# Performance work log

Hardware: AMD Instinct MI355X
Metric: run time of the kernel (lower is better)

## Reference

```python
import jax, jax.numpy as jnp
import numpy as np

INPUT_DIM = 2048
CLASSES = 1000
BATCH = 8192


def setup_inputs() -> dict:
    key = jax.random.key(0)
    kx, ky, kwx, kbx, kwy, kby = jax.random.split(key, 6)
    s_in = 1.0 / np.sqrt(INPUT_DIM)
    return {
        "x": jax.random.normal(kx, (BATCH, INPUT_DIM), dtype=jnp.float32),
        "y": jax.random.normal(ky, (BATCH, INPUT_DIM), dtype=jnp.float32),
        "Wx": jax.random.uniform(kwx, (CLASSES, INPUT_DIM), jnp.float32, -s_in, s_in),
        "bx": jax.random.uniform(kbx, (CLASSES,), jnp.float32, -s_in, s_in),
        "Wy": jax.random.uniform(kwy, (CLASSES, INPUT_DIM), jnp.float32, -s_in, s_in),
        "by": jax.random.uniform(kby, (CLASSES,), jnp.float32, -s_in, s_in),
    }


def _ds_combin_two(alpha1, alpha2, classes):
    # alpha1, alpha2: [B, C] Dirichlet params
    S1 = jnp.sum(alpha1, axis=1, keepdims=True)  # [B,1]
    S2 = jnp.sum(alpha2, axis=1, keepdims=True)
    b1 = (alpha1 - 1.0) / S1                      # belief masses [B,C]
    b2 = (alpha2 - 1.0) / S2
    u1 = classes / S1                             # uncertainty [B,1]
    u2 = classes / S2
    # bb_sum = sum_{i,j} b1_i b2_j = (sum b1)(sum b2); bb_diag = sum_i b1_i b2_i
    bb_sum = jnp.sum(b1, axis=1) * jnp.sum(b2, axis=1)   # [B]
    bb_diag = jnp.sum(b1 * b2, axis=1)                    # [B]
    C = (bb_sum - bb_diag)[:, None]                       # conflict [B,1]
    denom = 1.0 - C
    b_a = (b1 * b2 + b1 * u2 + b2 * u1) / denom           # [B,C]
    u_a = (u1 * u2) / denom                               # [B,1]
    S_a = classes / u_a                                   # [B,1]
    return b_a * S_a + 1.0                                # alpha_a [B,C]


def reference(x, y, Wx, bx, Wy, by):
    out_x = x @ Wx.T + bx                 # [B,C]
    out_y = y @ Wy.T + by
    alpha_x = jax.nn.softplus(out_x) + 1.0
    alpha_y = jax.nn.softplus(out_y) + 1.0
    alpha_a = _ds_combin_two(alpha_x, alpha_y, CLASSES)
    return (alpha_a, alpha_x, alpha_y)
```

## Files before the change

### kernel.cpp

```cpp
#include <hip/hip_runtime.h>
#include <hip/hip_bf16.h>
#include <math.h>

#define BATCH_N 8192
#define K_DIM   2048
#define CLS     1000

typedef __attribute__((ext_vector_type(8))) short short8;
typedef __attribute__((ext_vector_type(8))) unsigned short ushort8;
typedef __attribute__((ext_vector_type(4))) float floatx4;

static __device__ __forceinline__ float softplus_fast(float z) {
    return fmaxf(z, 0.f) + __logf(1.f + __expf(-fabsf(z)));
}


constexpr int NT = K_DIM / 32;

#define BARX  __builtin_amdgcn_s_barrier()
#define LGKM0 asm volatile("s_waitcnt lgkmcnt(0)" ::: "memory")
#define SB0   __builtin_amdgcn_sched_barrier(0)
#define PRIO1 __builtin_amdgcn_s_setprio(1)
#define PRIO0 __builtin_amdgcn_s_setprio(0)

__global__ __launch_bounds__(512, 2)
void gemm_fused(const float* __restrict__ Xa, const float* __restrict__ Xb,
                const float* __restrict__ Wa, const float* __restrict__ Wb,
                const float* __restrict__ biasa, const float* __restrict__ biasb,
                float* __restrict__ outa, float* __restrict__ outb)
{
    int flat = blockIdx.x + 4 * (blockIdx.y + 32 * blockIdx.z);
    int sw   = (flat & 7) * 32 + (flat >> 3);
    const int bx = sw & 3, by = (sw >> 2) & 31, bz = sw >> 7;

    const float* A    = bz ? Xb : Xa;
    const float* B    = bz ? Wb : Wa;
    const float* bias = bz ? biasb : biasa;
    float* out        = bz ? outb : outa;

    __shared__ ushort As[2][256 * 32];
    __shared__ ushort Bs[2][256 * 32];

    const int tid  = threadIdx.x;
    const int lane = tid & 63;
    const int wid  = tid >> 6;
    const int wr = wid >> 2, wc = wid & 3;
    const int fr = lane & 15, fg = lane >> 4;
    const int brow = by * 256;
    const int bcol = bx * 256;

    size_t a_g[2], b_g[2];
    int    l_of[2];
#pragma unroll
    for (int i = 0; i < 2; ++i) {
        int q = tid + i * 512;
        int p = q >> 3, c8 = q & 7, c8l = c8 ^ (p & 7);
        int r = 2 * p + (c8l >> 2);
        int k = (c8l & 3) * 8;
        a_g[i] = (size_t)(brow + r) * K_DIM + k;
        int wrow = bcol + r; if (wrow >= CLS) wrow = CLS - 1;
        b_g[i] = (size_t)wrow * K_DIM + k;
        l_of[i] = q * 8;
    }

    int afoff[8], bfoff[4];
#pragma unroll
    for (int m = 0; m < 8; ++m) {
        int row = wr * 128 + m * 16 + fr;
        int p = row >> 1;
        int c = (((row & 1) << 2) | fg) ^ (p & 7);
        afoff[m] = (p * 8 + c) * 8;
    }
#pragma unroll
    for (int n = 0; n < 4; ++n) {
        int row = wc * 64 + n * 16 + fr;
        int p = row >> 1;
        int c = (((row & 1) << 2) | fg) ^ (p & 7);
        bfoff[n] = (p * 8 + c) * 8;
    }

    floatx4 acc[8][4];
#pragma unroll
    for (int m = 0; m < 8; ++m)
#pragma unroll
        for (int n = 0; n < 4; ++n)
            acc[m][n] = (floatx4){0.f, 0.f, 0.f, 0.f};

    float4 ga[2][2], gb[2][2];

#define LOADT(t_) {                                                           \
    const size_t kb_ = (size_t)(t_) * 32;                                     \
    ga[0][0] = *(const float4*)(A + a_g[0] + kb_);                            \
    ga[0][1] = *(const float4*)(A + a_g[0] + kb_ + 4);                        \
    ga[1][0] = *(const float4*)(A + a_g[1] + kb_);                            \
    ga[1][1] = *(const float4*)(A + a_g[1] + kb_ + 4);                        \
    gb[0][0] = *(const float4*)(B + b_g[0] + kb_);                            \
    gb[0][1] = *(const float4*)(B + b_g[0] + kb_ + 4);                        \
    gb[1][0] = *(const float4*)(B + b_g[1] + kb_);                            \
    gb[1][1] = *(const float4*)(B + b_g[1] + kb_ + 4);                        \
}

#define CVTW(sl_) {                                                           \
    _Pragma("unroll")                                                         \
    for (int i = 0; i < 2; ++i) {                                             \
        ushort8 ta, tb;                                                       \
        _Pragma("unroll")                                                     \
        for (int j = 0; j < 4; ++j) {                                         \
            ta[j]     = __hip_bfloat16_raw(__float2bfloat16(((const float*)&ga[i][0])[j])).x; \
            ta[j + 4] = __hip_bfloat16_raw(__float2bfloat16(((const float*)&ga[i][1])[j])).x; \
            tb[j]     = __hip_bfloat16_raw(__float2bfloat16(((const float*)&gb[i][0])[j])).x; \
            tb[j + 4] = __hip_bfloat16_raw(__float2bfloat16(((const float*)&gb[i][1])[j])).x; \
        }                                                                     \
        *(ushort8*)&As[sl_][l_of[i]] = ta;                                    \
        *(ushort8*)&Bs[sl_][l_of[i]] = tb;                                    \
    }                                                                         \
}

    LOADT(0)
    CVTW(0)
    LOADT(1)
    SB0; LGKM0; BARX; SB0;

#pragma unroll 1
    for (int t = 0; t < NT; ++t) {
        const ushort* asl = &As[t & 1][0];
        const ushort* bsl = &Bs[t & 1][0];
        short8 af[8], bf[4];
#pragma unroll
        for (int m = 0; m < 8; ++m) af[m] = *(const short8*)(asl + afoff[m]);
#pragma unroll
        for (int n = 0; n < 4; ++n) bf[n] = *(const short8*)(bsl + bfoff[n]);

        PRIO1;
#pragma unroll
        for (int m = 0; m < 8; ++m)
#pragma unroll
            for (int n = 0; n < 4; ++n)
                acc[m][n] = __builtin_amdgcn_mfma_f32_16x16x32_bf16(
                    af[m], bf[n], acc[m][n], 0, 0, 0);
        PRIO0;

        if (t + 1 < NT) CVTW((t + 1) & 1)
        if (t + 2 < NT) LOADT(t + 2)
        SB0; LGKM0; BARX; SB0;
    }

#pragma unroll
    for (int n = 0; n < 4; ++n) {
        int col = bcol + wc * 64 + n * 16 + fr;
        if (col >= CLS) continue;
        float bv = bias[col];
#pragma unroll
        for (int m = 0; m < 8; ++m) {
#pragma unroll
            for (int j = 0; j < 4; ++j) {
                int row = brow + wr * 128 + m * 16 + fg * 4 + j;
                float z = acc[m][n][j] + bv;
                out[(size_t)row * CLS + col] = softplus_fast(z) + 1.f;
            }
        }
    }
}


__global__ __launch_bounds__(256)
void ds_combine(const float* __restrict__ AX, const float* __restrict__ AY,
                float* __restrict__ out)
{
    const int row = blockIdx.x * 4 + (threadIdx.x >> 6);
    const int l = threadIdx.x & 63;
    const float* ax = AX + (size_t)row * CLS;
    const float* ay = AY + (size_t)row * CLS;

    float4 vx[4], vy[4];
    float sx = 0.f, sy = 0.f, sp = 0.f;
#pragma unroll
    for (int c = 0; c < 4; ++c) {
        int idx = l + c * 64;
        if (idx < CLS / 4) {
            vx[c] = *(const float4*)(ax + idx * 4);
            vy[c] = *(const float4*)(ay + idx * 4);
            const float* px = (const float*)&vx[c];
            const float* py = (const float*)&vy[c];
#pragma unroll
            for (int j = 0; j < 4; ++j) {
                sx += px[j]; sy += py[j];
                sp += (px[j] - 1.f) * (py[j] - 1.f);
            }
        }
    }
#pragma unroll
    for (int off = 1; off < 64; off <<= 1) {
        sx += __shfl_xor(sx, off);
        sy += __shfl_xor(sy, off);
        sp += __shfl_xor(sp, off);
    }
    const float S1 = sx, S2 = sy, P = sp;
    const float i1 = 1.f / S1, i2 = 1.f / S2;
    const float u1 = (float)CLS * i1, u2 = (float)CLS * i2;
    const float sb1 = (S1 - (float)CLS) * i1;
    const float sb2 = (S2 - (float)CLS) * i2;
    const float conf = sb1 * sb2 - P * i1 * i2;
    const float denom = 1.f - conf;
    const float idenom = 1.f / denom;
    const float Sa = (float)CLS * denom / (u1 * u2);

#pragma unroll
    for (int c = 0; c < 4; ++c) {
        int idx = l + c * 64;
        if (idx < CLS / 4) {
            float4 vo;
            const float* px = (const float*)&vx[c];
            const float* py = (const float*)&vy[c];
            float* po = (float*)&vo;
#pragma unroll
            for (int j = 0; j < 4; ++j) {
                float b1 = (px[j] - 1.f) * i1;
                float b2 = (py[j] - 1.f) * i2;
                float ba = (b1 * b2 + b1 * u2 + b2 * u1) * idenom;
                po[j] = ba * Sa + 1.f;
            }
            *(float4*)(out + (size_t)row * CLS + idx * 4) = vo;
        }
    }
}

extern "C" void kernel_launch(void* const* d_in, const int* in_sizes, int n_in,
                              void* d_out, int out_size, void* d_ws, size_t ws_size,
                              hipStream_t stream) {
    const float* x  = (const float*)d_in[0];
    const float* y  = (const float*)d_in[1];
    const float* Wx = (const float*)d_in[2];
    const float* bx = (const float*)d_in[3];
    const float* Wy = (const float*)d_in[4];
    const float* by = (const float*)d_in[5];
    float* out = (float*)d_out;
    float* ax = out + (size_t)BATCH_N * CLS;
    float* ay = ax  + (size_t)BATCH_N * CLS;

    gemm_fused<<<dim3(4, 32, 2), 512, 0, stream>>>(
        x, y, Wx, Wy, bx, by, ax, ay);
    ds_combine<<<BATCH_N / 4, 256, 0, stream>>>(ax, ay, out);
}
```

Measured before the change: 109.8 us.

## Pre-convert weights to swizzled bf16 image and stream B via direct global-to-LDS loads

```diff
diff --git a/kernel.cpp b/kernel.cpp
--- a/kernel.cpp
+++ b/kernel.cpp
@@ -14,14 +14,197 @@
     return fmaxf(z, 0.f) + __logf(1.f + __expf(-fabsf(z)));
 }
 
-
-constexpr int NT = K_DIM / 32;
+static __device__ __forceinline__ void gld_lds16(const void* g, void* l) {
+    __builtin_amdgcn_global_load_lds(
+        (const __attribute__((address_space(1))) void*)g,
+        (__attribute__((address_space(3))) void*)l, 16, 0, 0);
+}
+
+static __device__ __forceinline__ ushort f2bfr(float f) {
+    return __hip_bfloat16_raw(__float2bfloat16(f)).x;
+}
 
 #define BARX  __builtin_amdgcn_s_barrier()
 #define LGKM0 asm volatile("s_waitcnt lgkmcnt(0)" ::: "memory")
+#define VMW(n) asm volatile("s_waitcnt vmcnt(" #n ")" ::: "memory")
 #define SB0   __builtin_amdgcn_sched_barrier(0)
 #define PRIO1 __builtin_amdgcn_s_setprio(1)
 #define PRIO0 __builtin_amdgcn_s_setprio(0)
+
+constexpr int NT = K_DIM / 32;
+
+__global__ __launch_bounds__(256)
+void make_wimg(const float* __restrict__ wx, const float* __restrict__ wy,
+               ushort* __restrict__ imgx, ushort* __restrict__ imgy)
+{
+    const float* src = blockIdx.z ? wy : wx;
+    ushort* dst      = blockIdx.z ? imgy : imgx;
+    int c = blockIdx.x * 256 + threadIdx.x;
+    int q  = c & 1023;
+    int t  = (c >> 10) & 63;
+    int bx = c >> 16;
+    int p = q >> 3, c8 = q & 7, c8l = c8 ^ (p & 7);
+    int r = 2 * p + (c8l >> 2);
+    int k = (c8l & 3) * 8 + t * 32;
+    int row = bx * 256 + r;
+    ushort8 v = (ushort8)0;
+    if (row < CLS) {
+        float4 a = *(const float4*)(src + (size_t)row * K_DIM + k);
+        float4 b = *(const float4*)(src + (size_t)row * K_DIM + k + 4);
+#pragma unroll
+        for (int j = 0; j < 4; ++j) {
+            v[j]     = f2bfr(((const float*)&a)[j]);
+            v[j + 4] = f2bfr(((const float*)&b)[j]);
+        }
+    }
+    *(ushort8*)(dst + (size_t)c * 8) = v;
+}
+
+__global__ __launch_bounds__(512, 2)
+void gemm_fused2(const float* __restrict__ Xa, const float* __restrict__ Xb,
+                 const ushort* __restrict__ imgx, const ushort* __restrict__ imgy,
+                 const float* __restrict__ biasa, const float* __restrict__ biasb,
+                 float* __restrict__ outa, float* __restrict__ outb)
+{
+    int flat = blockIdx.x + 4 * (blockIdx.y + 32 * blockIdx.z);
+    int sw   = (flat & 7) * 32 + (flat >> 3);
+    const int bx = sw & 3, by = (sw >> 2) & 31, bz = sw >> 7;
+
+    const float* A     = bz ? Xb : Xa;
+    const ushort* Wimg = bz ? imgy : imgx;
+    const float* bias  = bz ? biasb : biasa;
+    float* out         = bz ? outb : outa;
+
+    __shared__ ushort As[2][256 * 32];
+    __shared__ ushort Bs[2][256 * 32];
+
+    const int tid  = threadIdx.x;
+    const int lane = tid & 63;
+    const int wid  = tid >> 6;
+    const int wr = wid >> 2, wc = wid & 3;
+    const int fr = lane & 15, fg = lane >> 4;
+    const int brow = by * 256;
+    const int bcol = bx * 256;
+
+    size_t a_g[2];
+    int    l_of[2];
+#pragma unroll
+    for (int i = 0; i < 2; ++i) {
+        int q = tid + i * 512;
+        int p = q >> 3, c8 = q & 7, c8l = c8 ^ (p & 7);
+        int r = 2 * p + (c8l >> 2);
+        a_g[i] = (size_t)(brow + r) * K_DIM + (c8l & 3) * 8;
+        l_of[i] = q * 8;
+    }
+    const ushort* wbase = Wimg + (size_t)bx * 64 * 1024 * 8;
+
+    int afoff[8], bfoff[4];
+#pragma unroll
+    for (int m = 0; m < 8; ++m) {
+        int row = wr * 128 + m * 16 + fr;
+        int p = row >> 1;
+        int c = (((row & 1) << 2) | fg) ^ (p & 7);
+        afoff[m] = (p * 8 + c) * 8;
+    }
+#pragma unroll
+    for (int n = 0; n < 4; ++n) {
+        int row = wc * 64 + n * 16 + fr;
+        int p = row >> 1;
+        int c = (((row & 1) << 2) | fg) ^ (p & 7);
+        bfoff[n] = (p * 8 + c) * 8;
+    }
+
+    floatx4 acc[8][4];
+#pragma unroll
+    for (int m = 0; m < 8; ++m)
+#pragma unroll
+        for (int n = 0; n < 4; ++n)
+            acc[m][n] = (floatx4){0.f, 0.f, 0.f, 0.f};
+
+    float4 ga[2][2];
+
+#define LOADT(t_) {                                                           \
+    const size_t kb_ = (size_t)(t_) * 32;                                     \
+    ga[0][0] = *(const float4*)(A + a_g[0] + kb_);                            \
+    ga[0][1] = *(const float4*)(A + a_g[0] + kb_ + 4);                        \
+    ga[1][0] = *(const float4*)(A + a_g[1] + kb_);                            \
+    ga[1][1] = *(const float4*)(A + a_g[1] + kb_ + 4);                        \
+}
+
+#define CVTW(sl_) {                                                           \
+    _Pragma("unroll")                                                         \
+    for (int i = 0; i < 2; ++i) {                                             \
+        ushort8 ta;                                                           \
+        _Pragma("unroll")                                                     \
+        for (int j = 0; j < 4; ++j) {                                         \
+            ta[j]     = f2bfr(((const float*)&ga[i][0])[j]);                  \
+            ta[j + 4] = f2bfr(((const float*)&ga[i][1])[j]);                  \
+        }                                                                     \
+        *(ushort8*)&As[sl_][l_of[i]] = ta;                                    \
+    }                                                                         \
+}
+
+#define STAGE_B(t_) {                                                         \
+    const ushort* s_ = wbase + (size_t)(t_) * 1024 * 8;                       \
+    gld_lds16(s_ + (size_t)tid * 8,         &Bs[(t_) & 1][tid * 8]);          \
+    gld_lds16(s_ + (size_t)(tid + 512) * 8, &Bs[(t_) & 1][(tid + 512) * 8]); \
+}
+
+    STAGE_B(0)
+    LOADT(0)
+    CVTW(0)
+    LOADT(1)
+    VMW(8);
+    LGKM0; BARX; SB0;
+
+#pragma unroll 1
+    for (int t = 0; t < NT; ++t) {
+        if (t + 1 < NT) STAGE_B(t + 1)
+        SB0;
+
+        const ushort* asl = &As[t & 1][0];
+        const ushort* bsl = &Bs[t & 1][0];
+        short8 af[8], bf[4];
+#pragma unroll
+        for (int m = 0; m < 8; ++m) af[m] = *(const short8*)(asl + afoff[m]);
+#pragma unroll
+        for (int n = 0; n < 4; ++n) bf[n] = *(const short8*)(bsl + bfoff[n]);
+
+        PRIO1;
+#pragma unroll
+        for (int m = 0; m < 8; ++m)
+#pragma unroll
+            for (int n = 0; n < 4; ++n)
+                acc[m][n] = __builtin_amdgcn_mfma_f32_16x16x32_bf16(
+                    af[m], bf[n], acc[m][n], 0, 0, 0);
+        PRIO0;
+
+        if (t + 1 < NT) CVTW((t + 1) & 1)
+        if (t + 2 < NT) LOADT(t + 2)
+        SB0;
+        if (t + 1 < NT) {
+            if (t + 2 < NT) { VMW(8); }
+            else           { VMW(0); }
+            LGKM0; BARX; SB0;
+        }
+    }
+
+#pragma unroll
+    for (int n = 0; n < 4; ++n) {
+        int col = bcol + wc * 64 + n * 16 + fr;
+        if (col >= CLS) continue;
+        float bv = bias[col];
+#pragma unroll
+        for (int m = 0; m < 8; ++m) {
+#pragma unroll
+            for (int j = 0; j < 4; ++j) {
+                int row = brow + wr * 128 + m * 16 + fg * 4 + j;
+                float z = acc[m][n][j] + bv;
+                out[(size_t)row * CLS + col] = softplus_fast(z) + 1.f;
+            }
+        }
+    }
+}
 
 __global__ __launch_bounds__(512, 2)
 void gemm_fused(const float* __restrict__ Xa, const float* __restrict__ Xb,
@@ -88,7 +271,7 @@
 
     float4 ga[2][2], gb[2][2];
 
-#define LOADT(t_) {                                                           \
+#define FLOADT(t_) {                                                          \
     const size_t kb_ = (size_t)(t_) * 32;                                     \
     ga[0][0] = *(const float4*)(A + a_g[0] + kb_);                            \
     ga[0][1] = *(const float4*)(A + a_g[0] + kb_ + 4);                        \
@@ -99,26 +282,25 @@
     gb[1][0] = *(const float4*)(B + b_g[1] + kb_);                            \
     gb[1][1] = *(const float4*)(B + b_g[1] + kb_ + 4);                        \
 }
-
-#define CVTW(sl_) {                                                           \
+#define FCVTW(sl_) {                                                          \
     _Pragma("unroll")                                                         \
     for (int i = 0; i < 2; ++i) {                                             \
         ushort8 ta, tb;                                                       \
         _Pragma("unroll")                                                     \
         for (int j = 0; j < 4; ++j) {                                         \
-            ta[j]     = __hip_bfloat16_raw(__float2bfloat16(((const float*)&ga[i][0])[j])).x; \
-            ta[j + 4] = __hip_bfloat16_raw(__float2bfloat16(((const float*)&ga[i][1])[j])).x; \
-            tb[j]     = __hip_bfloat16_raw(__float2bfloat16(((const float*)&gb[i][0])[j])).x; \
-            tb[j + 4] = __hip_bfloat16_raw(__float2bfloat16(((const float*)&gb[i][1])[j])).x; \
+            ta[j]     = f2bfr(((const float*)&ga[i][0])[j]);                  \
+            ta[j + 4] = f2bfr(((const float*)&ga[i][1])[j]);                  \
+            tb[j]     = f2bfr(((const float*)&gb[i][0])[j]);                  \
+            tb[j + 4] = f2bfr(((const float*)&gb[i][1])[j]);                  \
         }                                                                     \
         *(ushort8*)&As[sl_][l_of[i]] = ta;                                    \
         *(ushort8*)&Bs[sl_][l_of[i]] = tb;                                    \
     }                                                                         \
 }
 
-    LOADT(0)
-    CVTW(0)
-    LOADT(1)
+    FLOADT(0)
+    FCVTW(0)
+    FLOADT(1)
     SB0; LGKM0; BARX; SB0;
 
 #pragma unroll 1
@@ -140,8 +322,8 @@
                     af[m], bf[n], acc[m][n], 0, 0, 0);
         PRIO0;
 
-        if (t + 1 < NT) CVTW((t + 1) & 1)
-        if (t + 2 < NT) LOADT(t + 2)
+        if (t + 1 < NT) FCVTW((t + 1) & 1)
+        if (t + 2 < NT) FLOADT(t + 2)
         SB0; LGKM0; BARX; SB0;
     }
 
@@ -238,7 +420,18 @@
     float* ax = out + (size_t)BATCH_N * CLS;
     float* ay = ax  + (size_t)BATCH_N * CLS;
 
-    gemm_fused<<<dim3(4, 32, 2), 512, 0, stream>>>(
-        x, y, Wx, Wy, bx, by, ax, ay);
+    const size_t IMG = (size_t)4 * 64 * 1024 * 8;
+    const size_t need = 2 * IMG * sizeof(ushort);
+
+    if (ws_size >= need) {
+        ushort* imgx = (ushort*)d_ws;
+        ushort* imgy = imgx + IMG;
+        make_wimg<<<dim3(1024, 1, 2), 256, 0, stream>>>(Wx, Wy, imgx, imgy);
+        gemm_fused2<<<dim3(4, 32, 2), 512, 0, stream>>>(
+            x, y, imgx, imgy, bx, by, ax, ay);
+    } else {
+        gemm_fused<<<dim3(4, 32, 2), 512, 0, stream>>>(
+            x, y, Wx, Wy, bx, by, ax, ay);
+    }
     ds_combine<<<BATCH_N / 4, 256, 0, stream>>>(ax, ay, out);
 }
```

After: 132.3 us. +20.5%, slower.

## Deepen GEMM LDS pipeline to four stages with one barrier per two tiles

Applied to the files above, without the earlier changes.

```diff
diff --git a/kernel.cpp b/kernel.cpp
--- a/kernel.cpp
+++ b/kernel.cpp
@@ -14,14 +14,18 @@
     return fmaxf(z, 0.f) + __logf(1.f + __expf(-fabsf(z)));
 }
 
-
-constexpr int NT = K_DIM / 32;
+static __device__ __forceinline__ ushort f2bfr(float f) {
+    return __hip_bfloat16_raw(__float2bfloat16(f)).x;
+}
 
 #define BARX  __builtin_amdgcn_s_barrier()
 #define LGKM0 asm volatile("s_waitcnt lgkmcnt(0)" ::: "memory")
 #define SB0   __builtin_amdgcn_sched_barrier(0)
 #define PRIO1 __builtin_amdgcn_s_setprio(1)
 #define PRIO0 __builtin_amdgcn_s_setprio(0)
+
+constexpr int NT = K_DIM / 32;
+
 
 __global__ __launch_bounds__(512, 2)
 void gemm_fused(const float* __restrict__ Xa, const float* __restrict__ Xb,
@@ -38,8 +42,8 @@
     const float* bias = bz ? biasb : biasa;
     float* out        = bz ? outb : outa;
 
-    __shared__ ushort As[2][256 * 32];
-    __shared__ ushort Bs[2][256 * 32];
+    __shared__ ushort As[4][256 * 32];
+    __shared__ ushort Bs[4][256 * 32];
 
     const int tid  = threadIdx.x;
     const int lane = tid & 63;
@@ -106,42 +110,50 @@
         ushort8 ta, tb;                                                       \
         _Pragma("unroll")                                                     \
         for (int j = 0; j < 4; ++j) {                                         \
-            ta[j]     = __hip_bfloat16_raw(__float2bfloat16(((const float*)&ga[i][0])[j])).x; \
-            ta[j + 4] = __hip_bfloat16_raw(__float2bfloat16(((const float*)&ga[i][1])[j])).x; \
-            tb[j]     = __hip_bfloat16_raw(__float2bfloat16(((const float*)&gb[i][0])[j])).x; \
-            tb[j + 4] = __hip_bfloat16_raw(__float2bfloat16(((const float*)&gb[i][1])[j])).x; \
+            ta[j]     = f2bfr(((const float*)&ga[i][0])[j]);                  \
+            ta[j + 4] = f2bfr(((const float*)&ga[i][1])[j]);                  \
+            tb[j]     = f2bfr(((const float*)&gb[i][0])[j]);                  \
+            tb[j + 4] = f2bfr(((const float*)&gb[i][1])[j]);                  \
         }                                                                     \
         *(ushort8*)&As[sl_][l_of[i]] = ta;                                    \
         *(ushort8*)&Bs[sl_][l_of[i]] = tb;                                    \
     }                                                                         \
 }
 
+#define COMPUTE(t_) {                                                         \
+    const ushort* asl = &As[(t_) & 3][0];                                     \
+    const ushort* bsl = &Bs[(t_) & 3][0];                                     \
+    short8 af[8], bf[4];                                                      \
+    _Pragma("unroll")                                                         \
+    for (int m = 0; m < 8; ++m) af[m] = *(const short8*)(asl + afoff[m]);     \
+    _Pragma("unroll")                                                         \
+    for (int n = 0; n < 4; ++n) bf[n] = *(const short8*)(bsl + bfoff[n]);     \
+    PRIO1;                                                                    \
+    _Pragma("unroll")                                                         \
+    for (int m = 0; m < 8; ++m)                                               \
+        _Pragma("unroll")                                                     \
+        for (int n = 0; n < 4; ++n)                                           \
+            acc[m][n] = __builtin_amdgcn_mfma_f32_16x16x32_bf16(              \
+                af[m], bf[n], acc[m][n], 0, 0, 0);                            \
+    PRIO0;                                                                    \
+}
+
     LOADT(0)
     CVTW(0)
     LOADT(1)
+    CVTW(1)
+    LOADT(2)
     SB0; LGKM0; BARX; SB0;
 
 #pragma unroll 1
-    for (int t = 0; t < NT; ++t) {
-        const ushort* asl = &As[t & 1][0];
-        const ushort* bsl = &Bs[t & 1][0];
-        short8 af[8], bf[4];
-#pragma unroll
-        for (int m = 0; m < 8; ++m) af[m] = *(const short8*)(asl + afoff[m]);
-#pragma unroll
-        for (int n = 0; n < 4; ++n) bf[n] = *(const short8*)(bsl + bfoff[n]);
-
-        PRIO1;
-#pragma unroll
-        for (int m = 0; m < 8; ++m)
-#pragma unroll
-            for (int n = 0; n < 4; ++n)
-                acc[m][n] = __builtin_amdgcn_mfma_f32_16x16x32_bf16(
-                    af[m], bf[n], acc[m][n], 0, 0, 0);
-        PRIO0;
-
-        if (t + 1 < NT) CVTW((t + 1) & 1)
-        if (t + 2 < NT) LOADT(t + 2)
+    for (int s = 0; s < NT / 2; ++s) {
+        const int t0 = 2 * s, t1 = 2 * s + 1;
+        COMPUTE(t0)
+        if (t0 + 2 < NT) CVTW((t0 + 2) & 3)
+        if (t0 + 3 < NT) LOADT(t0 + 3)
+        COMPUTE(t1)
+        if (t1 + 2 < NT) CVTW((t1 + 2) & 3)
+        if (t1 + 3 < NT) LOADT(t1 + 3)
         SB0; LGKM0; BARX; SB0;
     }
 
```

Result: slower. 117.1 us (+6.7%).
